# Performance work log

Hardware: AMD Instinct MI355X
Metric: run time of the kernel (lower is better)

## Reference

```python
import jax, jax.numpy as jnp
import numpy as np

B, S, D, P = 4, 2048, 1024, 1024

def setup_inputs() -> dict:
    key = jax.random.key(0)
    k1, k2, k3, k4 = jax.random.split(key, 4)
    x = jax.random.normal(k1, (B, S, D), dtype=jnp.float32)
    # nn.Linear weight is (out, in); store transposed (in, out) for x @ W
    scale = 1.0 / np.sqrt(D)
    Wq = jax.random.normal(k2, (D, P), dtype=jnp.float32) * scale
    Wk = jax.random.normal(k3, (D, P), dtype=jnp.float32) * scale
    Wv = jax.random.normal(k4, (D, P), dtype=jnp.float32) * scale
    return {"x": x, "Wq": Wq, "Wk": Wk, "Wv": Wv}

def reference(x, Wq, Wk, Wv):
    # projections (no bias)
    q = x @ Wq  # (B,S,P)
    k = x @ Wk
    v = x @ Wv
    scores = jnp.einsum('bsd,btd->bst', q, k)  # (B,S,S)
    seq = x.shape[1]
    causal = jnp.triu(jnp.ones((seq, seq), dtype=bool), k=1)
    scores = jnp.where(causal, -jnp.inf, scores)
    scores = scores / jnp.sqrt(jnp.asarray(P, dtype=scores.dtype))
    attn = jax.nn.softmax(scores, axis=-1)
    # dropout_prob=0.0 -> identity
    context = jnp.einsum('bst,btd->bsd', attn, v)  # (B,S,P)
    return context
```

## Files before the change

### kernel.cpp

```cpp
#include <hip/hip_runtime.h>
#include <hip/hip_bf16.h>


#define BDIM 4
#define SDIM 2048
#define DDIM 1024
#define PDIM 1024

typedef __attribute__((ext_vector_type(8))) short bf16x8;
typedef __attribute__((ext_vector_type(4))) float f32x4;

__device__ __forceinline__ unsigned short f2bf(float f) {
    union { float f; unsigned int u; } v; v.f = f;
    unsigned int u = v.u;
    unsigned int r = (u + 0x7fffu + ((u >> 16) & 1u)) >> 16;
    return (unsigned short)r;
}

__device__ __forceinline__ float bf2f(unsigned short h) {
    union { unsigned int u; float f; } v;
    v.u = ((unsigned int)h) << 16;
    return v.f;
}

__device__ __forceinline__ void async16(const unsigned short* g, unsigned short* l) {
    __builtin_amdgcn_global_load_lds(
        (const __attribute__((address_space(1))) unsigned int*)g,
        (__attribute__((address_space(3))) unsigned int*)l,
        16, 0, 0);
}

__device__ __forceinline__ void storeC(float* C, size_t idx, float v) { C[idx] = v; }
__device__ __forceinline__ void storeC(unsigned short* C, size_t idx, float v) { C[idx] = f2bf(v); }

__global__ __launch_bounds__(256) void cast_x_kernel(const float* __restrict__ x,
                                                     unsigned short* __restrict__ y) {
    int i = blockIdx.x * 256 + threadIdx.x;
    float4 v = ((const float4*)x)[i];
    ushort4 o;
    o.x = f2bf(v.x); o.y = f2bf(v.y); o.z = f2bf(v.z); o.w = f2bf(v.w);
    ((ushort4*)y)[i] = o;
}

__global__ __launch_bounds__(256) void transpose_cast_w(const float* __restrict__ W0,
                                                        const float* __restrict__ W1,
                                                        const float* __restrict__ W2,
                                                        unsigned short* __restrict__ T) {
    const float* W = (blockIdx.z == 0) ? W0 : (blockIdx.z == 1) ? W1 : W2;
    unsigned short* Tz = T + (size_t)blockIdx.z * DDIM * PDIM;
    __shared__ float t[32][33];
    int c0 = blockIdx.x * 32, r0 = blockIdx.y * 32;
    for (int i = threadIdx.y; i < 32; i += 8)
        t[i][threadIdx.x] = W[(size_t)(r0 + i) * PDIM + c0 + threadIdx.x];
    __syncthreads();
    for (int i = threadIdx.y; i < 32; i += 8)
        Tz[(size_t)(c0 + i) * DDIM + r0 + threadIdx.x] = f2bf(t[threadIdx.x][i]);
}

__global__ __launch_bounds__(256) void transpose_u16(const unsigned short* __restrict__ in,
                                                     int ldin, long long strideInZ,
                                                     unsigned short* __restrict__ out,
                                                     int ldout, long long strideOutZ) {
    __shared__ unsigned short t[32][33];
    in += (long long)blockIdx.z * strideInZ;
    out += (long long)blockIdx.z * strideOutZ;
    int c0 = blockIdx.x * 32, r0 = blockIdx.y * 32;
    for (int i = threadIdx.y; i < 32; i += 8)
        t[i][threadIdx.x] = in[(size_t)(r0 + i) * ldin + c0 + threadIdx.x];
    __syncthreads();
    for (int i = threadIdx.y; i < 32; i += 8)
        out[(size_t)(c0 + i) * ldout + r0 + threadIdx.x] = t[threadIdx.x][i];
}

template <typename CT>
__global__ __launch_bounds__(256) void gemm_bt(const unsigned short* __restrict__ A0,
                                               const unsigned short* __restrict__ A1,
                                               long long sA, int lda,
                                               const unsigned short* __restrict__ B0,
                                               long long sB, int ldb,
                                               CT* __restrict__ C0, CT* __restrict__ C1,
                                               long long sC, int ldc,
                                               int M, int N, int K, float alpha, int mode) {
    const int BM = 128, BN = 128, BK = 64;
    __shared__ __attribute__((aligned(16))) unsigned short As[BM * BK];
    __shared__ __attribute__((aligned(16))) unsigned short Bs[BN * BK];

    int tm = blockIdx.y * BM;
    int tn = blockIdx.x * BN;
    if (mode == 1 && tn > tm) return;
    int kend = (mode == 2) ? min(K, tm + BM) : K;

    int z = blockIdx.z;
    const unsigned short* A = (z < 2 ? A0 : A1) + (long long)(z & 1) * sA;
    const unsigned short* Bt = B0 + (long long)z * sB;
    CT* C = (z < 2 ? C0 : C1) + (long long)(z & 1) * sC;

    int tid  = threadIdx.x;
    int lane = tid & 63;
    int wave = tid >> 6;
    int wr   = (wave >> 1) * 64;
    int wc   = (wave & 1) * 64;
    int quad = lane >> 4;
    int l16  = lane & 15;
    int rsw  = l16 & 7;

    f32x4 acc[4][4] = {};

    int srow = tid >> 3;
    int scol = ((tid & 7) ^ (srow & 7)) * 8;
    const unsigned short* Ag = A + (size_t)(tm + srow) * lda + scol;
    const unsigned short* Bg = Bt + (size_t)(tn + srow) * ldb + scol;
    unsigned short* la = As + tid * 8;
    unsigned short* lb = Bs + tid * 8;
    const size_t pA = (size_t)32 * lda;
    const size_t pB = (size_t)32 * ldb;

    for (int k0 = 0; k0 < kend; k0 += BK) {
        async16(Ag + k0, la);
        async16(Ag + k0 + pA, la + 2048);
        async16(Ag + k0 + 2 * pA, la + 4096);
        async16(Ag + k0 + 3 * pA, la + 6144);
        async16(Bg + k0, lb);
        async16(Bg + k0 + pB, lb + 2048);
        async16(Bg + k0 + 2 * pB, lb + 4096);
        async16(Bg + k0 + 3 * pB, lb + 6144);
        __syncthreads();

#pragma unroll
        for (int s = 0; s < 2; s++) {
            int chunk = ((s * 4 + quad) ^ rsw) * 8;
            bf16x8 af[4], bfr[4];
#pragma unroll
            for (int i = 0; i < 4; i++)
                af[i] = *(const bf16x8*)(As + (wr + i * 16 + l16) * BK + chunk);
#pragma unroll
            for (int j = 0; j < 4; j++)
                bfr[j] = *(const bf16x8*)(Bs + (wc + j * 16 + l16) * BK + chunk);
#pragma unroll
            for (int i = 0; i < 4; i++)
#pragma unroll
                for (int j = 0; j < 4; j++)
                    acc[i][j] = __builtin_amdgcn_mfma_f32_16x16x32_bf16(af[i], bfr[j], acc[i][j], 0, 0, 0);
        }
        __syncthreads();
    }

#pragma unroll
    for (int i = 0; i < 4; i++) {
        int r0 = tm + wr + i * 16 + quad * 4;
#pragma unroll
        for (int j = 0; j < 4; j++) {
            int c = tn + wc + j * 16 + l16;
#pragma unroll
            for (int rr = 0; rr < 4; rr++) {
                int r = r0 + rr;
                float v = acc[i][j][rr] * alpha;
                if (mode == 1 && c > r) v = -1e30f;
                storeC(C, (size_t)r * ldc + c, v);
            }
        }
    }
}

__global__ __launch_bounds__(256) void softmax_causal(unsigned short* __restrict__ S01,
                                                      unsigned short* __restrict__ S23,
                                                      long long sS) {
    int row = blockIdx.x;
    int b = blockIdx.y;
    unsigned short* srow = (b < 2 ? S01 : S23) + (long long)(b & 1) * sS + (size_t)row * SDIM;
    int tid = threadIdx.x;
    int j0 = tid * 8;
    int valid = row + 1;
    __shared__ float red[4];

    bf16x8 v8 = *(const bf16x8*)(srow + j0);
    float f[8];
#pragma unroll
    for (int i = 0; i < 8; i++) f[i] = bf2f((unsigned short)v8[i]);

    float m = -1e30f;
#pragma unroll
    for (int i = 0; i < 8; i++) if (j0 + i < valid) m = fmaxf(m, f[i]);
#pragma unroll
    for (int o = 32; o; o >>= 1) m = fmaxf(m, __shfl_xor(m, o, 64));
    if ((tid & 63) == 0) red[tid >> 6] = m;
    __syncthreads();
    m = fmaxf(fmaxf(red[0], red[1]), fmaxf(red[2], red[3]));
    __syncthreads();

    float e[8];
    float l = 0.f;
#pragma unroll
    for (int i = 0; i < 8; i++) {
        e[i] = (j0 + i < valid) ? __expf(f[i] - m) : 0.f;
        l += e[i];
    }
#pragma unroll
    for (int o = 32; o; o >>= 1) l += __shfl_xor(l, o, 64);
    if ((tid & 63) == 0) red[tid >> 6] = l;
    __syncthreads();
    l = red[0] + red[1] + red[2] + red[3];
    float inv = 1.0f / l;

    bf16x8 o8;
#pragma unroll
    for (int i = 0; i < 8; i++) o8[i] = (short)f2bf(e[i] * inv);
    *(bf16x8*)(srow + j0) = o8;
}

extern "C" void kernel_launch(void* const* d_in, const int* in_sizes, int n_in,
                              void* d_out, int out_size, void* d_ws, size_t ws_size,
                              hipStream_t stream) {
    const float* x  = (const float*)d_in[0];
    const float* Wq = (const float*)d_in[1];
    const float* Wk = (const float*)d_in[2];
    const float* Wv = (const float*)d_in[3];
    float* out = (float*)d_out;

    const size_t MS = (size_t)BDIM * SDIM;
    const long long SS = (long long)SDIM * SDIM;
    char* ws = (char*)d_ws;
    size_t off = 0;
    unsigned short* Xb   = (unsigned short*)(ws + off);
    unsigned short* S01  = Xb;                          off += MS * DDIM * 2;
    unsigned short* WT   = (unsigned short*)(ws + off); off += 3ull * DDIM * PDIM * 2;
    unsigned short* QKVf = (unsigned short*)(ws + off); off += MS * 3ull * PDIM * 2;
    unsigned short* VT   = (unsigned short*)(ws + off); off += MS * PDIM * 2;
    unsigned short* S23  = (unsigned short*)(ws + off); off += 2ull * SS * 2;

    const int LQKV = 3 * PDIM;

    cast_x_kernel<<<(MS * DDIM) / 1024, 256, 0, stream>>>(x, Xb);

    transpose_cast_w<<<dim3(PDIM / 32, DDIM / 32, 3), dim3(32, 8), 0, stream>>>(Wq, Wk, Wv, WT);

    gemm_bt<unsigned short><<<dim3(LQKV / 128, MS / 128, 1), 256, 0, stream>>>(
        Xb, Xb, 0, DDIM, WT, 0, DDIM,
        QKVf, QKVf, 0, LQKV, (int)MS, LQKV, DDIM, 1.0f, 0);

    transpose_u16<<<dim3(PDIM / 32, SDIM / 32, BDIM), dim3(32, 8), 0, stream>>>(
        QKVf + 2 * PDIM, LQKV, (long long)SDIM * LQKV,
        VT, SDIM, (long long)PDIM * SDIM);

    const long long sQK = (long long)SDIM * LQKV;
    const float alpha = 1.0f / 32.0f;

    gemm_bt<unsigned short><<<dim3(SDIM / 128, SDIM / 128, BDIM), 256, 0, stream>>>(
        QKVf, QKVf + 2 * sQK, sQK, LQKV,
        QKVf + PDIM, sQK, LQKV,
        S01, S23, SS, SDIM, SDIM, SDIM, PDIM, alpha, 1);

    softmax_causal<<<dim3(SDIM, BDIM), 256, 0, stream>>>(S01, S23, SS);

    const long long sOut = (long long)SDIM * PDIM;
    gemm_bt<float><<<dim3(PDIM / 128, SDIM / 128, BDIM), 256, 0, stream>>>(
        S01, S23, SS, SDIM,
        VT, (long long)PDIM * SDIM, SDIM,
        out, out + 2 * sOut, sOut, PDIM, SDIM, PDIM, SDIM, 1.0f, 2);
}
```

Before: 270.2 us.

## Fuse V transpose into QKV GEMM epilogue, compact causal grid, templatize strides

The QKV projection GEMM now writes Q and K into separate contiguous buffers. It writes V transposed directly through an LDS staging tile in its epilogue, which removes the separate transpose_u16 kernel and its global round trip. The QK^T GEMM launches only the lower-triangular tiles (136 blocks per batch) by decoding a triangular index, so blocks that would exit immediately are never launched. Leading dimensions and K are now template constants, which allows full K-loop unrolling and constant address math. The V epilogue adds extra syncs and LDS traffic inside the GEMM.

```diff
diff --git a/kernel.cpp b/kernel.cpp
--- a/kernel.cpp
+++ b/kernel.cpp
@@ -57,38 +57,32 @@
         Tz[(size_t)(c0 + i) * DDIM + r0 + threadIdx.x] = f2bf(t[threadIdx.x][i]);
 }
 
-__global__ __launch_bounds__(256) void transpose_u16(const unsigned short* __restrict__ in,
-                                                     int ldin, long long strideInZ,
-                                                     unsigned short* __restrict__ out,
-                                                     int ldout, long long strideOutZ) {
-    __shared__ unsigned short t[32][33];
-    in += (long long)blockIdx.z * strideInZ;
-    out += (long long)blockIdx.z * strideOutZ;
-    int c0 = blockIdx.x * 32, r0 = blockIdx.y * 32;
-    for (int i = threadIdx.y; i < 32; i += 8)
-        t[i][threadIdx.x] = in[(size_t)(r0 + i) * ldin + c0 + threadIdx.x];
-    __syncthreads();
-    for (int i = threadIdx.y; i < 32; i += 8)
-        out[(size_t)(c0 + i) * ldout + r0 + threadIdx.x] = t[threadIdx.x][i];
-}
-
-template <typename CT>
-__global__ __launch_bounds__(256) void gemm_bt(const unsigned short* __restrict__ A0,
-                                               const unsigned short* __restrict__ A1,
-                                               long long sA, int lda,
-                                               const unsigned short* __restrict__ B0,
-                                               long long sB, int ldb,
-                                               CT* __restrict__ C0, CT* __restrict__ C1,
-                                               long long sC, int ldc,
-                                               int M, int N, int K, float alpha, int mode) {
+template <int LDA, int LDB, int LDC, int KMAX, int MODE, typename CT>
+__global__ __launch_bounds__(256) void gemm_bt(
+    const unsigned short* __restrict__ A0, const unsigned short* __restrict__ A1,
+    long long sA,
+    const unsigned short* __restrict__ B0, long long sB,
+    CT* __restrict__ C0, CT* __restrict__ C1, long long sC,
+    unsigned short* __restrict__ Kb, unsigned short* __restrict__ VT,
+    float alpha) {
     const int BM = 128, BN = 128, BK = 64;
-    __shared__ __attribute__((aligned(16))) unsigned short As[BM * BK];
-    __shared__ __attribute__((aligned(16))) unsigned short Bs[BN * BK];
-
-    int tm = blockIdx.y * BM;
-    int tn = blockIdx.x * BN;
-    if (mode == 1 && tn > tm) return;
-    int kend = (mode == 2) ? min(K, tm + BM) : K;
+    __shared__ __attribute__((aligned(16))) unsigned short smem[BM * BK + BN * BK];
+    unsigned short* As = smem;
+    unsigned short* Bs = smem + BM * BK;
+
+    int tm, tn;
+    if (MODE == 1) {
+        int i = blockIdx.x;
+        int t = (int)((sqrtf(8.f * i + 1.f) - 1.f) * 0.5f);
+        if ((t + 1) * (t + 2) / 2 <= i) t++;
+        if (t * (t + 1) / 2 > i) t--;
+        tm = t * BM;
+        tn = (i - t * (t + 1) / 2) * BN;
+    } else {
+        tm = blockIdx.y * BM;
+        tn = blockIdx.x * BN;
+    }
+    int kend = (MODE == 2) ? min(KMAX, tm + BM) : KMAX;
 
     int z = blockIdx.z;
     const unsigned short* A = (z < 2 ? A0 : A1) + (long long)(z & 1) * sA;
@@ -108,22 +102,20 @@
 
     int srow = tid >> 3;
     int scol = ((tid & 7) ^ (srow & 7)) * 8;
-    const unsigned short* Ag = A + (size_t)(tm + srow) * lda + scol;
-    const unsigned short* Bg = Bt + (size_t)(tn + srow) * ldb + scol;
+    const unsigned short* Ag = A + (size_t)(tm + srow) * LDA + scol;
+    const unsigned short* Bg = Bt + (size_t)(tn + srow) * LDB + scol;
     unsigned short* la = As + tid * 8;
     unsigned short* lb = Bs + tid * 8;
-    const size_t pA = (size_t)32 * lda;
-    const size_t pB = (size_t)32 * ldb;
-
-    for (int k0 = 0; k0 < kend; k0 += BK) {
+
+    auto kstep = [&](int k0) {
         async16(Ag + k0, la);
-        async16(Ag + k0 + pA, la + 2048);
-        async16(Ag + k0 + 2 * pA, la + 4096);
-        async16(Ag + k0 + 3 * pA, la + 6144);
+        async16(Ag + k0 + 32 * LDA, la + 2048);
+        async16(Ag + k0 + 64 * LDA, la + 4096);
+        async16(Ag + k0 + 96 * LDA, la + 6144);
         async16(Bg + k0, lb);
-        async16(Bg + k0 + pB, lb + 2048);
-        async16(Bg + k0 + 2 * pB, lb + 4096);
-        async16(Bg + k0 + 3 * pB, lb + 6144);
+        async16(Bg + k0 + 32 * LDB, lb + 2048);
+        async16(Bg + k0 + 64 * LDB, lb + 4096);
+        async16(Bg + k0 + 96 * LDB, lb + 6144);
         __syncthreads();
 
 #pragma unroll
@@ -143,20 +135,86 @@
                     acc[i][j] = __builtin_amdgcn_mfma_f32_16x16x32_bf16(af[i], bfr[j], acc[i][j], 0, 0, 0);
         }
         __syncthreads();
+    };
+
+    if constexpr (MODE != 2) {
+#pragma unroll
+        for (int k0 = 0; k0 < KMAX; k0 += BK) kstep(k0);
+    } else {
+        for (int k0 = 0; k0 < kend; k0 += 2 * BK) { kstep(k0); kstep(k0 + BK); }
     }
 
-#pragma unroll
-    for (int i = 0; i < 4; i++) {
-        int r0 = tm + wr + i * 16 + quad * 4;
-#pragma unroll
-        for (int j = 0; j < 4; j++) {
-            int c = tn + wc + j * 16 + l16;
-#pragma unroll
-            for (int rr = 0; rr < 4; rr++) {
-                int r = r0 + rr;
-                float v = acc[i][j][rr] * alpha;
-                if (mode == 1 && c > r) v = -1e30f;
-                storeC(C, (size_t)r * ldc + c, v);
+    if constexpr (MODE == 0) {
+        if (tn < 2048) {
+            unsigned short* D = (tn < 1024 ? (unsigned short*)C0 : Kb);
+            int cbase = tn & 1023;
+#pragma unroll
+            for (int i = 0; i < 4; i++) {
+                int r0 = tm + wr + i * 16 + quad * 4;
+#pragma unroll
+                for (int j = 0; j < 4; j++) {
+                    int c = cbase + wc + j * 16 + l16;
+#pragma unroll
+                    for (int rr = 0; rr < 4; rr++)
+                        D[(size_t)(r0 + rr) * 1024 + c] = f2bf(acc[i][j][rr]);
+                }
+            }
+        } else {
+            int b = tm >> 11;
+            int s0 = tm & 2047;
+            unsigned short* VTb = VT + (size_t)b * (PDIM * SDIM)
+                                     + (size_t)(tn - 2048) * SDIM + s0;
+            const int TP = 136;
+            unsigned short* T = smem;
+#pragma unroll
+            for (int p = 0; p < 4; p++) {
+                int jbase = -1;
+                if (wc == 0 && p == 0) jbase = 0;
+                if (wc == 0 && p == 1) jbase = 2;
+                if (wc == 64 && p == 2) jbase = 0;
+                if (wc == 64 && p == 3) jbase = 2;
+                if (jbase >= 0) {
+#pragma unroll
+                    for (int jj = 0; jj < 2; jj++) {
+                        int j = jbase + jj;
+                        int c = (wc + j * 16 + l16) - 32 * p;
+#pragma unroll
+                        for (int i = 0; i < 4; i++) {
+                            int r = wr + i * 16 + quad * 4;
+                            ushort4 w;
+                            w.x = f2bf(acc[i][j][0]); w.y = f2bf(acc[i][j][1]);
+                            w.z = f2bf(acc[i][j][2]); w.w = f2bf(acc[i][j][3]);
+                            *(ushort4*)(T + c * TP + r) = w;
+                        }
+                    }
+                }
+                __syncthreads();
+                {
+                    int lr = tid >> 3;
+                    int ck = (tid & 7) * 16;
+                    bf16x8 u0 = *(const bf16x8*)(T + lr * TP + ck);
+                    bf16x8 u1 = *(const bf16x8*)(T + lr * TP + ck + 8);
+                    unsigned short* dst = VTb + (size_t)(32 * p + lr) * SDIM + ck;
+                    *(bf16x8*)(dst) = u0;
+                    *(bf16x8*)(dst + 8) = u1;
+                }
+                __syncthreads();
+            }
+        }
+    } else {
+#pragma unroll
+        for (int i = 0; i < 4; i++) {
+            int r0 = tm + wr + i * 16 + quad * 4;
+#pragma unroll
+            for (int j = 0; j < 4; j++) {
+                int c = tn + wc + j * 16 + l16;
+#pragma unroll
+                for (int rr = 0; rr < 4; rr++) {
+                    int r = r0 + rr;
+                    float v = acc[i][j][rr] * alpha;
+                    if (MODE == 1 && c > r) v = -1e30f;
+                    storeC(C, (size_t)r * LDC + c, v);
+                }
             }
         }
     }
@@ -224,37 +282,30 @@
     unsigned short* Xb   = (unsigned short*)(ws + off);
     unsigned short* S01  = Xb;                          off += MS * DDIM * 2;
     unsigned short* WT   = (unsigned short*)(ws + off); off += 3ull * DDIM * PDIM * 2;
-    unsigned short* QKVf = (unsigned short*)(ws + off); off += MS * 3ull * PDIM * 2;
+    unsigned short* Q    = (unsigned short*)(ws + off); off += MS * PDIM * 2;
+    unsigned short* Kb   = (unsigned short*)(ws + off); off += MS * PDIM * 2;
     unsigned short* VT   = (unsigned short*)(ws + off); off += MS * PDIM * 2;
     unsigned short* S23  = (unsigned short*)(ws + off); off += 2ull * SS * 2;
 
-    const int LQKV = 3 * PDIM;
-
     cast_x_kernel<<<(MS * DDIM) / 1024, 256, 0, stream>>>(x, Xb);
 
     transpose_cast_w<<<dim3(PDIM / 32, DDIM / 32, 3), dim3(32, 8), 0, stream>>>(Wq, Wk, Wv, WT);
 
-    gemm_bt<unsigned short><<<dim3(LQKV / 128, MS / 128, 1), 256, 0, stream>>>(
-        Xb, Xb, 0, DDIM, WT, 0, DDIM,
-        QKVf, QKVf, 0, LQKV, (int)MS, LQKV, DDIM, 1.0f, 0);
-
-    transpose_u16<<<dim3(PDIM / 32, SDIM / 32, BDIM), dim3(32, 8), 0, stream>>>(
-        QKVf + 2 * PDIM, LQKV, (long long)SDIM * LQKV,
-        VT, SDIM, (long long)PDIM * SDIM);
-
-    const long long sQK = (long long)SDIM * LQKV;
+    gemm_bt<DDIM, DDIM, PDIM, DDIM, 0, unsigned short>
+        <<<dim3(3 * PDIM / 128, MS / 128, 1), 256, 0, stream>>>(
+        Xb, Xb, 0, WT, 0, Q, Q, 0, Kb, VT, 1.0f);
+
+    const long long sQ = (long long)SDIM * PDIM;
     const float alpha = 1.0f / 32.0f;
 
-    gemm_bt<unsigned short><<<dim3(SDIM / 128, SDIM / 128, BDIM), 256, 0, stream>>>(
-        QKVf, QKVf + 2 * sQK, sQK, LQKV,
-        QKVf + PDIM, sQK, LQKV,
-        S01, S23, SS, SDIM, SDIM, SDIM, PDIM, alpha, 1);
+    gemm_bt<PDIM, PDIM, SDIM, PDIM, 1, unsigned short>
+        <<<dim3(136, 1, BDIM), 256, 0, stream>>>(
+        Q, Q + 2 * sQ, sQ, Kb, sQ, S01, S23, SS, nullptr, nullptr, alpha);
 
     softmax_causal<<<dim3(SDIM, BDIM), 256, 0, stream>>>(S01, S23, SS);
 
     const long long sOut = (long long)SDIM * PDIM;
-    gemm_bt<float><<<dim3(PDIM / 128, SDIM / 128, BDIM), 256, 0, stream>>>(
-        S01, S23, SS, SDIM,
-        VT, (long long)PDIM * SDIM, SDIM,
-        out, out + 2 * sOut, sOut, PDIM, SDIM, PDIM, SDIM, 1.0f, 2);
-}
+    gemm_bt<SDIM, SDIM, PDIM, SDIM, 2, float>
+        <<<dim3(PDIM / 128, SDIM / 128, BDIM), 256, 0, stream>>>(
+        S01, S23, SS, VT, sQ, out, out + 2 * sOut, sOut, nullptr, nullptr, 1.0f);
+}
```

Result: faster. 235.0 us (-13.0%).
